# Optimization experiments

Hardware: AMD Instinct MI355X
Metric: run time of the kernel (lower is better)

Reference implementation:

```python
import jax, jax.numpy as jnp
import numpy as np

H = 128          # hidden
L = 4            # num PNA layers
NG = 32          # graphs in the batch
OUT = 12
N_NODES = 30000
N_EDGES = 480000
IN_NODE = 64
IN_EDGE = 16
EPS_BN = 1e-5
EPS_STD = 1e-5
# deg histogram torch.tensor([1,2,3,4,5,6]): cnt_i nodes have degree i
_cnt = np.arange(1.0, 7.0)
AVG_LOG = float((np.log(np.arange(6) + 1.0) * _cnt).sum() / _cnt.sum())


def _lin(k, fan_in, fan_out):
    return jax.random.normal(k, (fan_in, fan_out), jnp.float32) * 0.05


def setup_inputs() -> dict:
    key = jax.random.key(0)
    ks = jax.random.split(key, 16)
    d = {}
    d["x"] = jax.random.normal(ks[0], (N_NODES, IN_NODE), jnp.float32)
    d["edge_attr"] = jax.random.normal(ks[1], (N_EDGES, IN_EDGE), jnp.float32)
    d["edge_index"] = jax.random.randint(ks[2], (2, N_EDGES), 0, N_NODES)
    d["batch"] = jnp.sort(jax.random.randint(ks[3], (N_NODES,), 0, NG))
    d["node_emb_W"] = _lin(ks[4], IN_NODE, H)
    d["node_emb_b"] = jnp.zeros((H,), jnp.float32)
    d["edge_emb_W"] = _lin(ks[5], IN_EDGE, H)
    d["edge_emb_b"] = jnp.zeros((H,), jnp.float32)
    kl = jax.random.split(ks[6], 4 * L)
    d["edge_enc_W"] = jnp.stack([_lin(kl[i], H, H) for i in range(L)])
    d["edge_enc_b"] = jnp.zeros((L, H), jnp.float32)
    d["pre_W"] = jnp.stack([_lin(kl[L + i], 3 * H, H) for i in range(L)])
    d["pre_b"] = jnp.zeros((L, H), jnp.float32)
    d["post_W"] = jnp.stack([_lin(kl[2 * L + i], 13 * H, H) for i in range(L)])
    d["post_b"] = jnp.zeros((L, H), jnp.float32)
    d["lin_W"] = jnp.stack([_lin(kl[3 * L + i], H, H) for i in range(L)])
    d["lin_b"] = jnp.zeros((L, H), jnp.float32)
    d["bn_gamma"] = jnp.ones((L, H), jnp.float32)
    d["bn_beta"] = jnp.zeros((L, H), jnp.float32)
    d["head1_W"] = _lin(ks[7], H, H // 2)
    d["head1_b"] = jnp.zeros((H // 2,), jnp.float32)
    d["head2_W"] = _lin(ks[8], H // 2, OUT)
    d["head2_b"] = jnp.zeros((OUT,), jnp.float32)
    return d


def _pna_layer(x, e, src, dst, eW, eb, pW, pb, oW, ob, lW, lb):
    n = x.shape[0]
    ee = e @ eW + eb                                      # edge encoder [E, H]
    h = jnp.concatenate([x[dst], x[src], ee], axis=-1)    # (x_i, x_j, e) [E, 3H]
    m = h @ pW + pb                                       # pre-nn messages [E, H]
    ones = jnp.ones((m.shape[0],), m.dtype)
    deg = jax.ops.segment_sum(ones, dst, num_segments=n)  # in-degree [N]
    degc = jnp.maximum(deg, 1.0)[:, None]
    has = (deg > 0.0)[:, None]
    mean = jax.ops.segment_sum(m, dst, num_segments=n) / degc
    mn = jnp.where(has, jax.ops.segment_min(m, dst, num_segments=n), 0.0)
    mx = jnp.where(has, jax.ops.segment_max(m, dst, num_segments=n), 0.0)
    mean_sq = jax.ops.segment_sum(m * m, dst, num_segments=n) / degc
    std = jnp.sqrt(jax.nn.relu(mean_sq - mean * mean) + EPS_STD)
    agg = jnp.concatenate([mean, mn, mx, std], axis=-1)   # aggregators [N, 4H]
    amp = jnp.log(degc + 1.0) / AVG_LOG                   # amplification scale
    out = jnp.concatenate([agg, agg * amp, agg / amp], axis=-1)  # id/amp/atten [N, 12H]
    out = jnp.concatenate([x, out], axis=-1) @ oW + ob    # post-nn [N, H]
    return out @ lW + lb                                  # final lin


def reference(x, edge_index, batch, edge_attr, node_emb_W, node_emb_b,
              edge_emb_W, edge_emb_b, edge_enc_W, edge_enc_b, pre_W, pre_b,
              post_W, post_b, lin_W, lin_b, bn_gamma, bn_beta,
              head1_W, head1_b, head2_W, head2_b):
    src, dst = edge_index[0], edge_index[1]
    h = x @ node_emb_W + node_emb_b
    e = edge_attr @ edge_emb_W + edge_emb_b
    for l in range(L):
        h = _pna_layer(h, e, src, dst, edge_enc_W[l], edge_enc_b[l],
                       pre_W[l], pre_b[l], post_W[l], post_b[l],
                       lin_W[l], lin_b[l])
        mu = h.mean(axis=0)
        var = h.var(axis=0)  # biased, as BatchNorm training-mode normalization
        h = (h - mu) / jnp.sqrt(var + EPS_BN) * bn_gamma[l] + bn_beta[l]
        h = jax.nn.relu(h)   # dropout == identity (eval mode reference)
    g = jax.ops.segment_sum(h, batch, num_segments=NG)   # global_add_pool [NG, H]
    z = jax.nn.relu(g @ head1_W + head1_b)
    return z @ head2_W + head2_b
```

## Files before the change

kernel.cpp:

```cpp
#include <hip/hip_runtime.h>
#include <hip/hip_bf16.h>
#include <math.h>

#define NN 30000
#define NE 480000
#define NLAYER 4
#define NGR 32
#define NOUT 12
#define EPS_BN 1e-5f
#define EPS_STD 1e-5f
#define AVG_LOG 1.3821454785305053f

typedef unsigned short ushort_t;
typedef __bf16 bf16x8 __attribute__((ext_vector_type(8)));
typedef float floatx4 __attribute__((ext_vector_type(4)));

__device__ __forceinline__ float bfu(ushort_t u){
  union { unsigned int ui; float f; } c; c.ui = ((unsigned int)u) << 16; return c.f;
}
__device__ __forceinline__ ushort_t f2bf(float f){
  union { float f; unsigned int u; } c; c.f = f;
  unsigned int lsb = (c.u >> 16) & 1u;
  c.u += 0x7FFFu + lsb;
  return (ushort_t)(c.u >> 16);
}

__device__ __forceinline__ int plausible(unsigned int bits32){
  unsigned int e = (bits32 >> 23) & 0xFF;
  if(e == 0xFF) return 0;
  if(bits32 == 0 || bits32 == 0x80000000u) return 1;
  return (e >= 93 && e <= 140) ? 1 : 0;
}

__global__ void k_detect(const ushort_t* __restrict__ xr, int* __restrict__ flag){
  __shared__ int cnt[2];
  if(threadIdx.x < 2) cnt[threadIdx.x] = 0;
  __syncthreads();
  const unsigned int* xf = (const unsigned int*)xr;
  int gf = 0, gb = 0;
  for(int i = threadIdx.x; i < 1024; i += 256){
    gf += plausible(xf[i]);
    gb += plausible(((unsigned int)xr[i]) << 16);
  }
  atomicAdd(&cnt[0], gf);
  atomicAdd(&cnt[1], gb);
  __syncthreads();
  if(threadIdx.x == 0) *flag = (cnt[1] >= cnt[0]) ? 1 : 0;
}

#define NJOBS 19
struct CvtJob { const void* s; float* d; int n; };
struct CvtArgs { CvtJob j[NJOBS]; const int* flag; };

__global__ void k_cvt(CvtArgs a){
  int ji = blockIdx.y;
  const int isbf = *a.flag;
  float* d = a.j[ji].d;
  int n = a.j[ji].n;
  if(isbf){
    const ushort_t* s = (const ushort_t*)a.j[ji].s;
    for(int i = blockIdx.x*256 + threadIdx.x; i < n; i += gridDim.x*256) d[i] = bfu(s[i]);
  } else {
    const float* s = (const float*)a.j[ji].s;
    for(int i = blockIdx.x*256 + threadIdx.x; i < n; i += gridDim.x*256) d[i] = s[i];
  }
}

__global__ void k_xbf(const void* __restrict__ x, ushort_t* __restrict__ d,
                      const int* __restrict__ flag){
  int i = blockIdx.x*256 + threadIdx.x;
  if(i >= NN*64) return;
  if(*flag) d[i] = ((const ushort_t*)x)[i];
  else      d[i] = f2bf(((const float*)x)[i]);
}

#define NTR 29
struct TrJob { const float* s; ushort_t* d; int K, N; };
struct TrArgs { TrJob j[NTR]; };

__global__ void k_tr(TrArgs a){
  TrJob j = a.j[blockIdx.y];
  int total = j.K * j.N;
  for(int i = blockIdx.x*256 + threadIdx.x; i < total; i += gridDim.x*256){
    int n = i / j.K, k = i % j.K;
    j.d[i] = f2bf(j.s[(size_t)k * j.N + n]);
  }
}

__global__ void k_deg(const int* __restrict__ dst, int* __restrict__ deg){
  int i = blockIdx.x*256 + threadIdx.x;
  if(i < NE){
    unsigned d = (unsigned)dst[i];
    if(d < NN) atomicAdd(&deg[d], 1);
  }
}

__global__ void k_scan(const int* __restrict__ deg, int* __restrict__ rp){
  __shared__ int wsum[16];
  __shared__ int carry;
  int tid = threadIdx.x, lane = tid & 63, wid = tid >> 6;
  if(tid==0){ carry = 0; rp[0] = 0; }
  __syncthreads();
  for(int base=0; base<NN; base+=1024){
    int i = base + tid;
    int v = (i<NN) ? deg[i] : 0;
    int incl = v;
    #pragma unroll
    for(int off=1; off<64; off<<=1){
      int t = __shfl_up(incl, off, 64);
      if(lane >= off) incl += t;
    }
    if(lane==63) wsum[wid] = incl;
    __syncthreads();
    int woff = 0;
    for(int wI=0; wI<wid; wI++) woff += wsum[wI];
    if(i<NN) rp[i+1] = carry + woff + incl;
    __syncthreads();
    if(tid==0){
      int t = 0;
      for(int wI=0; wI<16; wI++) t += wsum[wI];
      carry += t;
    }
    __syncthreads();
  }
}

__global__ void k_scatter(const int* __restrict__ src, const int* __restrict__ dst,
                          const int* __restrict__ rp, int* __restrict__ fill,
                          int* __restrict__ src_csr, int* __restrict__ eix_csr){
  int i = blockIdx.x*256 + threadIdx.x;
  if(i >= NE) return;
  unsigned d = (unsigned)dst[i];
  unsigned s = (unsigned)src[i];
  if(d >= NN || s >= NN) return;
  int pos = rp[d] + atomicAdd(&fill[d], 1);
  src_csr[pos] = (int)s;
  eix_csr[pos] = i;
}

__global__ void k_gather_ea(const int* __restrict__ eix, const void* __restrict__ ea,
                            float* __restrict__ out, const int* __restrict__ flag){
  int j = blockIdx.x*128 + threadIdx.x;
  if(j >= NE) return;
  int i = eix[j];
  float* d = out + (size_t)j*16;
  if(*flag){
    const ushort_t* s = (const ushort_t*)ea + (size_t)i*16;
    #pragma unroll
    for(int k=0;k<16;k++) d[k] = bfu(s[k]);
  } else {
    const float* s = (const float*)ea + (size_t)i*16;
    #pragma unroll
    for(int k=0;k<16;k++) d[k] = s[k];
  }
}

__global__ void k_prep_K(const float* __restrict__ embW, const float* __restrict__ embB,
                         const float* __restrict__ encW, const float* __restrict__ encB,
                         const float* __restrict__ preW, const float* __restrict__ preB,
                         float* __restrict__ Kf){
  int l = blockIdx.x, c = threadIdx.x;
  const float* eW = encW + (size_t)l*128*128;
  const float* P3 = preW + (size_t)l*384*128 + 256*128;
  __shared__ float tmp[17][128];
  for(int r=0;r<16;r++){
    float a = 0.f;
    for(int k=0;k<128;k++) a += embW[r*128+k]*eW[k*128+c];
    tmp[r][c] = a;
  }
  {
    float a = encB[l*128+c];
    for(int k=0;k<128;k++) a += embB[k]*eW[k*128+c];
    tmp[16][c] = a;
  }
  __syncthreads();
  float* o = Kf + (size_t)l*17*128;
  for(int r=0;r<16;r++){
    float a = 0.f;
    for(int k=0;k<128;k++) a += tmp[r][k]*P3[k*128+c];
    o[r*128+c] = a;
  }
  {
    float a = preB[l*128+c];
    for(int k=0;k<128;k++) a += tmp[16][k]*P3[k*128+c];
    o[16*128+c] = a;
  }
}

template<int EPI, int OUTBF>
__launch_bounds__(256)
__global__ void k_mm(const ushort_t* __restrict__ A, const ushort_t* __restrict__ BT,
                     void* __restrict__ C, int M, int K, int ldc,
                     const float* __restrict__ bias,
                     const float* __restrict__ Tm,
                     const float* __restrict__ ampv, const float* __restrict__ invv,
                     float* __restrict__ bnsum, float* __restrict__ bnsq){
  __shared__ __align__(16) ushort_t Als[128][88];
  __shared__ __align__(16) ushort_t Bls[128][88];
  __shared__ float s_sum[128];
  __shared__ float s_sq[128];
  const int tid = threadIdx.x;
  const int m0 = blockIdx.x*128, n0 = blockIdx.y*128;
  const int w = tid >> 6, lane = tid & 63;
  const int wm = (w & 1)*64, wn = (w >> 1)*64;
  const int quad = lane >> 4, l15 = lane & 15;
  floatx4 acc[4][4] = {};

  for(int k0=0; k0<K; k0+=64){
    #pragma unroll
    for(int i=0;i<4;i++){
      int c = tid + 256*i;
      int row = c >> 3, kc = (c & 7)*8;
      uint4 va = make_uint4(0u,0u,0u,0u);
      int gr = m0 + row;
      if(gr < M) va = *(const uint4*)(A + (size_t)gr*K + k0 + kc);
      *(uint4*)(&Als[row][kc]) = va;
      uint4 vb = *(const uint4*)(BT + (size_t)(n0+row)*K + k0 + kc);
      *(uint4*)(&Bls[row][kc]) = vb;
    }
    __syncthreads();
    #pragma unroll
    for(int ks=0; ks<64; ks+=32){
      bf16x8 a[4], b[4];
      #pragma unroll
      for(int i=0;i<4;i++) a[i] = *(const bf16x8*)(&Als[wm+16*i+l15][ks+quad*8]);
      #pragma unroll
      for(int j=0;j<4;j++) b[j] = *(const bf16x8*)(&Bls[wn+16*j+l15][ks+quad*8]);
      #pragma unroll
      for(int i=0;i<4;i++)
        #pragma unroll
        for(int j=0;j<4;j++)
          acc[i][j] = __builtin_amdgcn_mfma_f32_16x16x32_bf16(a[i], b[j], acc[i][j], 0, 0, 0);
    }
    __syncthreads();
  }

  float s[4] = {0,0,0,0}, q[4] = {0,0,0,0};
  if(EPI==2){
    if(tid < 128){ s_sum[tid] = 0.f; s_sq[tid] = 0.f; }
    __syncthreads();
  }
  #pragma unroll
  for(int i=0;i<4;i++){
    #pragma unroll
    for(int r=0;r<4;r++){
      int grow = m0 + wm + 16*i + quad*4 + r;
      if(grow >= M) continue;
      float amp = 0.f, iv = 0.f;
      const float* tr = nullptr;
      if(EPI==1){ amp = ampv[grow]; iv = invv[grow]; tr = Tm + (size_t)grow*384; }
      #pragma unroll
      for(int j=0;j<4;j++){
        int gcol = n0 + wn + 16*j + l15;
        float v = acc[i][j][r];
        if(bias) v += bias[gcol];
        if(EPI==1) v += tr[gcol] + amp*tr[128+gcol] + iv*tr[256+gcol];
        if(OUTBF) ((ushort_t*)C)[(size_t)grow*ldc + gcol] = f2bf(v);
        else      ((float*)  C)[(size_t)grow*ldc + gcol] = v;
        if(EPI==2){ s[j] += v; q[j] += v*v; }
      }
    }
  }
  if(EPI==2){
    #pragma unroll
    for(int j=0;j<4;j++){
      atomicAdd(&s_sum[wn + 16*j + l15], s[j]);
      atomicAdd(&s_sq [wn + 16*j + l15], q[j]);
    }
    __syncthreads();
    if(tid < 128){
      atomicAdd(&bnsum[n0 + tid], s_sum[tid]);
      atomicAdd(&bnsq [n0 + tid], s_sq[tid]);
    }
  }
}

__launch_bounds__(128)
__global__ void k_agg(const int* __restrict__ rp, const int* __restrict__ src_csr,
                      const float* __restrict__ ea_csr, const float* __restrict__ Kf,
                      const float* __restrict__ AB,
                      ushort_t* __restrict__ agg, float* __restrict__ ampv,
                      float* __restrict__ invv){
  const int n = blockIdx.x, c = threadIdx.x;
  const int s0 = rp[n], e0 = rp[n+1];
  const int deg = e0 - s0;
  float kcol[16];
  #pragma unroll
  for(int k=0;k<16;k++) kcol[k] = Kf[k*128+c];
  const float base = AB[(size_t)n*256 + c] + Kf[16*128+c];
  float sum=0.f, sq=0.f, mn=INFINITY, mx=-INFINITY;
  __shared__ float ea_s[16][16];
  __shared__ int src_s[16];
  for(int j0=s0; j0<e0; j0+=16){
    int cnt = min(16, e0-j0);
    __syncthreads();
    int ee = c>>4, kk = c&15;
    if(ee < cnt)   ea_s[ee][kk]   = ea_csr[(size_t)(j0+ee)*16+kk];
    if(ee+8 < cnt) ea_s[ee+8][kk] = ea_csr[(size_t)(j0+ee+8)*16+kk];
    if(c < cnt) src_s[c] = src_csr[j0+c];
    __syncthreads();
    for(int e=0;e<cnt;e++){
      float m = base + AB[(size_t)src_s[e]*256 + 128 + c];
      #pragma unroll
      for(int k=0;k<16;k++) m += ea_s[e][k]*kcol[k];
      sum += m; sq += m*m; mn = fminf(mn,m); mx = fmaxf(mx,m);
    }
  }
  float degc = (float)(deg>0?deg:1);
  float mean = sum/degc;
  float var  = fmaxf(sq/degc - mean*mean, 0.f);
  float sd = sqrtf(var + EPS_STD);
  if(deg==0){ mn=0.f; mx=0.f; }
  ushort_t* o = agg + (size_t)n*512;
  o[c]       = f2bf(mean);
  o[128+c]   = f2bf(mn);
  o[256+c]   = f2bf(mx);
  o[384+c]   = f2bf(sd);
  if(c==0){
    float amp = logf(degc+1.f)/AVG_LOG;
    ampv[n] = amp; invv[n] = 1.f/amp;
  }
}

__global__ void k_bn_fin(const float* __restrict__ bnsum, const float* __restrict__ bnsq,
                         const float* __restrict__ gamma, const float* __restrict__ beta,
                         float* __restrict__ scale, float* __restrict__ shift){
  int c = threadIdx.x;
  float mu  = bnsum[c]*(1.f/NN);
  float var = fmaxf(bnsq[c]*(1.f/NN) - mu*mu, 0.f);
  float inv = 1.f/sqrtf(var + EPS_BN);
  float sc = gamma[c]*inv;
  scale[c] = sc;
  shift[c] = beta[c] - mu*sc;
}

__global__ void k_bn_relu(const float* __restrict__ y, const float* __restrict__ scale,
                          const float* __restrict__ shift, ushort_t* __restrict__ h){
  int i = blockIdx.x*256 + threadIdx.x;
  if(i >= NN*128) return;
  int c = i & 127;
  float v = fmaxf(y[i]*scale[c] + shift[c], 0.f);
  h[i] = f2bf(v);
}

__launch_bounds__(128)
__global__ void k_pool(const ushort_t* __restrict__ h, const int* __restrict__ batch,
                       float* __restrict__ g){
  int c = threadIdx.x;
  int r0 = blockIdx.x*512;
  int r1 = min(r0+512, NN);
  int cur = batch[r0] & 31;
  float acc = 0.f;
  for(int r=r0;r<r1;r++){
    int b = batch[r] & 31;
    if(b != cur){ atomicAdd(&g[(size_t)cur*128+c], acc); acc=0.f; cur=b; }
    acc += bfu(h[(size_t)r*128+c]);
  }
  atomicAdd(&g[(size_t)cur*128+c], acc);
}

__launch_bounds__(256)
__global__ void k_head(const float* __restrict__ g, const float* __restrict__ W1,
                       const float* __restrict__ b1, const float* __restrict__ W2,
                       const float* __restrict__ b2, void* __restrict__ out,
                       const int* __restrict__ flag){
  __shared__ float gs[32][128];
  __shared__ float zs[32][64];
  int tid = threadIdx.x;
  for(int i=tid;i<32*128;i+=256) gs[i>>7][i&127] = g[i];
  __syncthreads();
  for(int i=tid;i<32*64;i+=256){
    int r=i>>6, c=i&63;
    float a = b1[c];
    for(int k=0;k<128;k++) a += gs[r][k]*W1[k*64+c];
    zs[r][c] = fmaxf(a, 0.f);
  }
  __syncthreads();
  const int isbf = *flag;
  for(int i=tid;i<NGR*NOUT;i+=256){
    int r = i/NOUT, c = i%NOUT;
    float a = b2[c];
    for(int k=0;k<64;k++) a += zs[r][k]*W2[k*12+c];
    if(isbf) ((ushort_t*)out)[i] = f2bf(a);
    else     ((float*)out)[i] = a;
  }
}

extern "C" void kernel_launch(void* const* d_in, const int* in_sizes, int n_in,
                              void* d_out, int out_size, void* d_ws, size_t ws_size,
                              hipStream_t stream){
  const void* x_raw = d_in[0];
  const void* ea_raw;
  const int*  eidx;
  const int*  batch;
  if(in_sizes[1] == 2*NE){
    eidx   = (const int*)d_in[1];
    batch  = (const int*)d_in[2];
    ea_raw = d_in[3];
  } else {
    ea_raw = d_in[1];
    eidx   = (const int*)d_in[2];
    batch  = (const int*)d_in[3];
  }
  const void* nembW_r = d_in[4];
  const void* nembB_r = d_in[5];
  const void* eembW_r = d_in[6];
  const void* eembB_r = d_in[7];
  const void* encW_r  = d_in[8];
  const void* encB_r  = d_in[9];
  const void* preW_r  = d_in[10];
  const void* preB_r  = d_in[11];
  const void* postW_r = d_in[12];
  const void* postB_r = d_in[13];
  const void* linW_r  = d_in[14];
  const void* linB_r  = d_in[15];
  const void* bnG_r   = d_in[16];
  const void* bnB_r   = d_in[17];
  const void* h1W_r   = d_in[18];
  const void* h1B_r   = d_in[19];
  const void* h2W_r   = d_in[20];
  const void* h2B_r   = d_in[21];

  char* p = (char*)d_ws;
  auto alloc = [&](size_t bytes)->void*{
    void* r = (void*)p; p += (bytes + 255) & ~(size_t)255; return r;
  };
  int*      dtflag  = (int*)     alloc(sizeof(int)*16);
  int*      deg     = (int*)     alloc(sizeof(int)*NN);
  int*      fill    = (int*)     alloc(sizeof(int)*NN);
  int*      rp      = (int*)     alloc(sizeof(int)*(NN+1));
  int*      src_csr = (int*)     alloc(sizeof(int)*NE);
  int*      eix_csr = (int*)     alloc(sizeof(int)*NE);
  float*    ea_csr  = (float*)   alloc(sizeof(float)*(size_t)NE*16);
  ushort_t* xbf     = (ushort_t*)alloc(sizeof(ushort_t)*(size_t)NN*64);
  ushort_t* h       = (ushort_t*)alloc(sizeof(ushort_t)*(size_t)NN*128);
  ushort_t* aggb    = (ushort_t*)alloc(sizeof(ushort_t)*(size_t)NN*512);
  ushort_t* z       = (ushort_t*)alloc(sizeof(ushort_t)*(size_t)NN*128);
  float*    AB      = (float*)   alloc(sizeof(float)*(size_t)NN*256);
  float*    Tm      = (float*)   alloc(sizeof(float)*(size_t)NN*384);
  float*    y       = (float*)   alloc(sizeof(float)*(size_t)NN*128);
  float*    ampv    = (float*)   alloc(sizeof(float)*NN);
  float*    invv    = (float*)   alloc(sizeof(float)*NN);
  float*    Kf      = (float*)   alloc(sizeof(float)*4*17*128);
  float*    bnstat  = (float*)   alloc(sizeof(float)*256);
  float*    bnscale = (float*)   alloc(sizeof(float)*128);
  float*    bnshift = (float*)   alloc(sizeof(float)*128);
  float*    g       = (float*)   alloc(sizeof(float)*32*128);
  ushort_t* WembT   = (ushort_t*)alloc(sizeof(ushort_t)*128*64);
  ushort_t* P12T    = (ushort_t*)alloc(sizeof(ushort_t)*4*256*128);
  ushort_t* WcatT   = (ushort_t*)alloc(sizeof(ushort_t)*(size_t)4*384*512);
  ushort_t* W0T     = (ushort_t*)alloc(sizeof(ushort_t)*4*128*128);
  ushort_t* linWT   = (ushort_t*)alloc(sizeof(ushort_t)*4*128*128);
  float* nembW = (float*)alloc(sizeof(float)*64*128);
  float* nembB = (float*)alloc(sizeof(float)*128);
  float* eembW = (float*)alloc(sizeof(float)*16*128);
  float* eembB = (float*)alloc(sizeof(float)*128);
  float* encW  = (float*)alloc(sizeof(float)*4*128*128);
  float* encB  = (float*)alloc(sizeof(float)*4*128);
  float* preW  = (float*)alloc(sizeof(float)*4*384*128);
  float* preB  = (float*)alloc(sizeof(float)*4*128);
  float* postW = (float*)alloc(sizeof(float)*(size_t)4*1664*128);
  float* postB = (float*)alloc(sizeof(float)*4*128);
  float* linW  = (float*)alloc(sizeof(float)*4*128*128);
  float* linB  = (float*)alloc(sizeof(float)*4*128);
  float* bnG   = (float*)alloc(sizeof(float)*4*128);
  float* bnB   = (float*)alloc(sizeof(float)*4*128);
  float* h1W   = (float*)alloc(sizeof(float)*128*64);
  float* h1B   = (float*)alloc(sizeof(float)*64);
  float* h2W   = (float*)alloc(sizeof(float)*64*12);
  float* h2B   = (float*)alloc(sizeof(float)*12);

  CvtArgs ca;
  ca.flag = dtflag;
  int ji = 0;
  auto job = [&](const void* s, float* d, int n){ ca.j[ji].s=s; ca.j[ji].d=d; ca.j[ji].n=n; ji++; };
  job(nembW_r, nembW, 64*128);
  job(nembB_r, nembB, 128);
  job(eembW_r, eembW, 16*128);
  job(eembB_r, eembB, 128);
  job(encW_r,  encW,  4*128*128);
  job(encB_r,  encB,  4*128);
  job(preW_r,  preW,  4*384*128);
  job(preB_r,  preB,  4*128);
  job(postW_r, postW, 4*1664*128);
  job(postB_r, postB, 4*128);
  job(linW_r,  linW,  4*128*128);
  job(linB_r,  linB,  4*128);
  job(bnG_r,   bnG,   4*128);
  job(bnB_r,   bnB,   4*128);
  job(h1W_r,   h1W,   128*64);
  job(h1B_r,   h1B,   64);
  job(h2W_r,   h2W,   64*12);
  job(h2B_r,   h2B,   12);
  job(h2B_r,   h2B,   12);

  TrArgs ta;
  int ti = 0;
  auto tj = [&](const float* s, ushort_t* d, int K, int N){ ta.j[ti].s=s; ta.j[ti].d=d; ta.j[ti].K=K; ta.j[ti].N=N; ti++; };
  tj(nembW, WembT, 64, 128);
  for(int l=0;l<4;l++){
    const float* pw = preW + (size_t)l*384*128;
    tj(pw,            P12T + (size_t)l*256*128,           128, 128);
    tj(pw + 128*128,  P12T + (size_t)l*256*128 + 128*128, 128, 128);
    const float* po = postW + (size_t)l*1664*128;
    for(int b=0;b<3;b++)
      tj(po + (size_t)(128 + b*512)*128, WcatT + (size_t)l*384*512 + (size_t)b*128*512, 512, 128);
    tj(po, W0T + (size_t)l*128*128, 128, 128);
    tj(linW + (size_t)l*128*128, linWT + (size_t)l*128*128, 128, 128);
  }

  const int* esrc = eidx;
  const int* edst = eidx + NE;

  hipMemsetAsync(deg, 0, sizeof(int)*NN, stream);
  hipMemsetAsync(fill, 0, sizeof(int)*NN, stream);
  hipMemsetAsync(g, 0, sizeof(float)*32*128, stream);

  k_detect<<<1, 256, 0, stream>>>((const ushort_t*)x_raw, dtflag);
  k_cvt<<<dim3(256, NJOBS), 256, 0, stream>>>(ca);
  k_xbf<<<(NN*64+255)/256, 256, 0, stream>>>(x_raw, xbf, dtflag);
  k_tr<<<dim3(32, NTR), 256, 0, stream>>>(ta);

  k_deg<<<(NE+255)/256, 256, 0, stream>>>(edst, deg);
  k_scan<<<1, 1024, 0, stream>>>(deg, rp);
  k_scatter<<<(NE+255)/256, 256, 0, stream>>>(esrc, edst, rp, fill, src_csr, eix_csr);
  k_gather_ea<<<(NE+127)/128, 128, 0, stream>>>(eix_csr, ea_raw, ea_csr, dtflag);
  k_prep_K<<<4, 128, 0, stream>>>(eembW, eembB, encW, encB, preW, preB, Kf);

  const int MB = (NN + 127)/128;

  k_mm<0,1><<<dim3(MB,1), 256, 0, stream>>>(xbf, WembT, h, NN, 64, 128,
                                            nembB, nullptr, nullptr, nullptr, nullptr, nullptr);

  for(int l=0; l<NLAYER; l++){
    k_mm<0,0><<<dim3(MB,2), 256, 0, stream>>>(h, P12T + (size_t)l*256*128, AB, NN, 128, 256,
                                              nullptr, nullptr, nullptr, nullptr, nullptr, nullptr);
    k_agg<<<NN, 128, 0, stream>>>(rp, src_csr, ea_csr, Kf + (size_t)l*17*128,
                                  AB, aggb, ampv, invv);
    k_mm<0,0><<<dim3(MB,3), 256, 0, stream>>>(aggb, WcatT + (size_t)l*384*512, Tm, NN, 512, 384,
                                              nullptr, nullptr, nullptr, nullptr, nullptr, nullptr);
    k_mm<1,1><<<dim3(MB,1), 256, 0, stream>>>(h, W0T + (size_t)l*128*128, z, NN, 128, 128,
                                              postB + l*128, Tm, ampv, invv, nullptr, nullptr);
    hipMemsetAsync(bnstat, 0, sizeof(float)*256, stream);
    k_mm<2,0><<<dim3(MB,1), 256, 0, stream>>>(z, linWT + (size_t)l*128*128, y, NN, 128, 128,
                                              linB + l*128, nullptr, nullptr, nullptr,
                                              bnstat, bnstat+128);
    k_bn_fin<<<1, 128, 0, stream>>>(bnstat, bnstat+128, bnG + l*128, bnB + l*128,
                                    bnscale, bnshift);
    k_bn_relu<<<(NN*128+255)/256, 256, 0, stream>>>(y, bnscale, bnshift, h);
  }

  k_pool<<<(NN+511)/512, 128, 0, stream>>>(h, batch, g);
  k_head<<<1, 256, 0, stream>>>(g, h1W, h1B, h2W, h2B, d_out, dtflag);
}
```

Baseline: 1.194 ms.

## Fold final linear into post weights, drop one GEMM per layer, parallelize setup

The final linear layer is folded into the post-NN weights and bias on the device, which removes one 128x128 GEMM and the intermediate z buffer in every layer. BatchNorm statistics move into the fused epilogue as per-block partial sums, replacing atomics and a memset. Several setup kernels are also restructured: a multi-block prefix scan, a tiled transpose, prep_K split across 68 blocks, pooling without atomics, and edge attributes stored in bf16. A per-node insertion sort keeps the CSR edge order deterministic, and folding the weights changes rounding slightly.

```diff
diff --git a/kernel.cpp b/kernel.cpp
--- a/kernel.cpp
+++ b/kernel.cpp
@@ -10,6 +10,7 @@
 #define EPS_BN 1e-5f
 #define EPS_STD 1e-5f
 #define AVG_LOG 1.3821454785305053f
+#define MB_GRID 235
 
 typedef unsigned short ushort_t;
 typedef __bf16 bf16x8 __attribute__((ext_vector_type(8)));
@@ -48,7 +49,7 @@
   if(threadIdx.x == 0) *flag = (cnt[1] >= cnt[0]) ? 1 : 0;
 }
 
-#define NJOBS 19
+#define NJOBS 18
 struct CvtJob { const void* s; float* d; int n; };
 struct CvtArgs { CvtJob j[NJOBS]; const int* flag; };
 
@@ -74,17 +75,76 @@
   else      d[i] = f2bf(((const float*)x)[i]);
 }
 
-#define NTR 29
+#define NTR 9
 struct TrJob { const float* s; ushort_t* d; int K, N; };
 struct TrArgs { TrJob j[NTR]; };
 
 __global__ void k_tr(TrArgs a){
   TrJob j = a.j[blockIdx.y];
-  int total = j.K * j.N;
-  for(int i = blockIdx.x*256 + threadIdx.x; i < total; i += gridDim.x*256){
-    int n = i / j.K, k = i % j.K;
-    j.d[i] = f2bf(j.s[(size_t)k * j.N + n]);
-  }
+  int nk = j.K >> 6, nn = j.N >> 6;
+  int tile = blockIdx.x;
+  if(tile >= nk*nn) return;
+  int tk = tile % nk, tn = tile / nk;
+  int k0 = tk*64, n0 = tn*64;
+  __shared__ float t[64][65];
+  int w = threadIdx.x >> 6, c = threadIdx.x & 63;
+  #pragma unroll
+  for(int i=0;i<16;i+=1){
+    int r = i*4 + w;
+    t[r][c] = j.s[(size_t)(k0+r)*j.N + n0 + c];
+  }
+  __syncthreads();
+  #pragma unroll
+  for(int i=0;i<16;i+=1){
+    int r = i*4 + w;
+    j.d[(size_t)(n0+r)*j.K + k0 + c] = f2bf(t[c][r]);
+  }
+}
+
+#define NFOLD 16
+struct FoldJob { const float* s1; const float* s2; ushort_t* d; int Kd; };
+struct FoldArgs { FoldJob j[NFOLD]; };
+
+__global__ void k_fold(FoldArgs a){
+  FoldJob j = a.j[blockIdx.y];
+  const int n0 = blockIdx.x*16;
+  __shared__ float s2s[128][16];
+  int tid = threadIdx.x;
+  for(int idx = tid; idx < 128*16; idx += 256){
+    int t = idx >> 4, jj = idx & 15;
+    s2s[t][jj] = j.s2[t*128 + n0 + jj];
+  }
+  __syncthreads();
+  for(int k = tid; k < j.Kd; k += 256){
+    float part[16];
+    #pragma unroll
+    for(int p=0;p<16;p++) part[p] = 0.f;
+    for(int t0=0; t0<128; t0+=32){
+      float rr[32];
+      #pragma unroll
+      for(int tt=0;tt<32;tt++) rr[tt] = j.s1[(size_t)k*128 + t0 + tt];
+      #pragma unroll
+      for(int p=0;p<16;p++){
+        float acc = 0.f;
+        #pragma unroll
+        for(int tt=0;tt<32;tt++) acc += rr[tt]*s2s[t0+tt][p];
+        part[p] += acc;
+      }
+    }
+    #pragma unroll
+    for(int p=0;p<16;p++)
+      j.d[(size_t)(n0+p)*j.Kd + k] = f2bf(part[p]);
+  }
+}
+
+__global__ void k_foldb(const float* __restrict__ postB, const float* __restrict__ linW,
+                        const float* __restrict__ linB, float* __restrict__ biasY){
+  int l = blockIdx.x, c = threadIdx.x;
+  float a = linB[l*128+c];
+  const float* L = linW + (size_t)l*128*128;
+  const float* pb = postB + l*128;
+  for(int t=0;t<128;t++) a += pb[t]*L[t*128+c];
+  biasY[l*128+c] = a;
 }
 
 __global__ void k_deg(const int* __restrict__ dst, int* __restrict__ deg){
@@ -95,34 +155,42 @@
   }
 }
 
-__global__ void k_scan(const int* __restrict__ deg, int* __restrict__ rp){
+__global__ void k_scan1(const int* __restrict__ deg, int* __restrict__ rp,
+                        int* __restrict__ bsum){
   __shared__ int wsum[16];
-  __shared__ int carry;
   int tid = threadIdx.x, lane = tid & 63, wid = tid >> 6;
-  if(tid==0){ carry = 0; rp[0] = 0; }
-  __syncthreads();
-  for(int base=0; base<NN; base+=1024){
-    int i = base + tid;
-    int v = (i<NN) ? deg[i] : 0;
-    int incl = v;
-    #pragma unroll
-    for(int off=1; off<64; off<<=1){
-      int t = __shfl_up(incl, off, 64);
-      if(lane >= off) incl += t;
-    }
-    if(lane==63) wsum[wid] = incl;
-    __syncthreads();
-    int woff = 0;
-    for(int wI=0; wI<wid; wI++) woff += wsum[wI];
-    if(i<NN) rp[i+1] = carry + woff + incl;
-    __syncthreads();
-    if(tid==0){
-      int t = 0;
-      for(int wI=0; wI<16; wI++) t += wsum[wI];
-      carry += t;
-    }
-    __syncthreads();
-  }
+  int i = blockIdx.x*1024 + tid;
+  int v = (i < NN) ? deg[i] : 0;
+  int incl = v;
+  #pragma unroll
+  for(int off=1; off<64; off<<=1){
+    int t = __shfl_up(incl, off, 64);
+    if(lane >= off) incl += t;
+  }
+  if(lane==63) wsum[wid] = incl;
+  __syncthreads();
+  int woff = 0;
+  for(int w=0; w<wid; w++) woff += wsum[w];
+  if(i < NN) rp[i+1] = incl + woff;
+  if(tid == 0){
+    int t = 0;
+    for(int w=0; w<16; w++) t += wsum[w];
+    bsum[blockIdx.x] = t;
+  }
+}
+
+__global__ void k_scan2(const int* __restrict__ bsum, int* __restrict__ boff,
+                        int* __restrict__ rp, int nb){
+  if(threadIdx.x == 0){
+    int run = 0;
+    for(int b=0;b<nb;b++){ boff[b] = run; run += bsum[b]; }
+    rp[0] = 0;
+  }
+}
+
+__global__ void k_scan3(int* __restrict__ rp, const int* __restrict__ boff){
+  int i = blockIdx.x*1024 + threadIdx.x;
+  if(i < NN) rp[i+1] += boff[blockIdx.x];
 }
 
 __global__ void k_scatter(const int* __restrict__ src, const int* __restrict__ dst,
@@ -138,20 +206,36 @@
   eix_csr[pos] = i;
 }
 
+__global__ void k_srt(const int* __restrict__ rp, int* __restrict__ eix,
+                      int* __restrict__ src){
+  int n = blockIdx.x*256 + threadIdx.x;
+  if(n >= NN) return;
+  int s0 = rp[n], e0 = rp[n+1];
+  for(int i=s0+1;i<e0;i++){
+    int ke = eix[i], ks = src[i];
+    int j = i-1;
+    while(j >= s0 && eix[j] > ke){
+      eix[j+1] = eix[j]; src[j+1] = src[j]; j--;
+    }
+    eix[j+1] = ke; src[j+1] = ks;
+  }
+}
+
 __global__ void k_gather_ea(const int* __restrict__ eix, const void* __restrict__ ea,
-                            float* __restrict__ out, const int* __restrict__ flag){
+                            ushort_t* __restrict__ out, const int* __restrict__ flag){
   int j = blockIdx.x*128 + threadIdx.x;
   if(j >= NE) return;
   int i = eix[j];
-  float* d = out + (size_t)j*16;
+  uint4* d = (uint4*)(out + (size_t)j*16);
   if(*flag){
-    const ushort_t* s = (const ushort_t*)ea + (size_t)i*16;
-    #pragma unroll
-    for(int k=0;k<16;k++) d[k] = bfu(s[k]);
+    const uint4* s = (const uint4*)((const ushort_t*)ea + (size_t)i*16);
+    d[0] = s[0]; d[1] = s[1];
   } else {
     const float* s = (const float*)ea + (size_t)i*16;
+    union { ushort_t us[16]; uint4 u4[2]; } pk;
     #pragma unroll
-    for(int k=0;k<16;k++) d[k] = s[k];
+    for(int k=0;k<16;k++) pk.us[k] = f2bf(s[k]);
+    d[0] = pk.u4[0]; d[1] = pk.u4[1];
   }
 }
 
@@ -159,32 +243,26 @@
                          const float* __restrict__ encW, const float* __restrict__ encB,
                          const float* __restrict__ preW, const float* __restrict__ preB,
                          float* __restrict__ Kf){
-  int l = blockIdx.x, c = threadIdx.x;
+  int bx = blockIdx.x;
+  int l = bx / 17, r = bx % 17;
+  int c = threadIdx.x;
   const float* eW = encW + (size_t)l*128*128;
   const float* P3 = preW + (size_t)l*384*128 + 256*128;
-  __shared__ float tmp[17][128];
-  for(int r=0;r<16;r++){
-    float a = 0.f;
-    for(int k=0;k<128;k++) a += embW[r*128+k]*eW[k*128+c];
-    tmp[r][c] = a;
-  }
-  {
-    float a = encB[l*128+c];
+  __shared__ float trow[128];
+  float a;
+  if(r < 16){
+    a = 0.f;
+    const float* w = embW + r*128;
+    for(int k=0;k<128;k++) a += w[k]*eW[k*128+c];
+  } else {
+    a = encB[l*128+c];
     for(int k=0;k<128;k++) a += embB[k]*eW[k*128+c];
-    tmp[16][c] = a;
-  }
-  __syncthreads();
-  float* o = Kf + (size_t)l*17*128;
-  for(int r=0;r<16;r++){
-    float a = 0.f;
-    for(int k=0;k<128;k++) a += tmp[r][k]*P3[k*128+c];
-    o[r*128+c] = a;
-  }
-  {
-    float a = preB[l*128+c];
-    for(int k=0;k<128;k++) a += tmp[16][k]*P3[k*128+c];
-    o[16*128+c] = a;
-  }
+  }
+  trow[c] = a;
+  __syncthreads();
+  float o = (r==16) ? preB[l*128+c] : 0.f;
+  for(int k=0;k<128;k++) o += trow[k]*P3[k*128+c];
+  Kf[(size_t)l*17*128 + r*128 + c] = o;
 }
 
 template<int EPI, int OUTBF>
@@ -194,11 +272,11 @@
                      const float* __restrict__ bias,
                      const float* __restrict__ Tm,
                      const float* __restrict__ ampv, const float* __restrict__ invv,
-                     float* __restrict__ bnsum, float* __restrict__ bnsq){
+                     float* __restrict__ bnpart){
   __shared__ __align__(16) ushort_t Als[128][88];
   __shared__ __align__(16) ushort_t Bls[128][88];
-  __shared__ float s_sum[128];
-  __shared__ float s_sq[128];
+  __shared__ float s_part[8][128];
+  __shared__ float q_part[8][128];
   const int tid = threadIdx.x;
   const int m0 = blockIdx.x*128, n0 = blockIdx.y*128;
   const int w = tid >> 6, lane = tid & 63;
@@ -236,10 +314,6 @@
   }
 
   float s[4] = {0,0,0,0}, q[4] = {0,0,0,0};
-  if(EPI==2){
-    if(tid < 128){ s_sum[tid] = 0.f; s_sq[tid] = 0.f; }
-    __syncthreads();
-  }
   #pragma unroll
   for(int i=0;i<4;i++){
     #pragma unroll
@@ -257,27 +331,31 @@
         if(EPI==1) v += tr[gcol] + amp*tr[128+gcol] + iv*tr[256+gcol];
         if(OUTBF) ((ushort_t*)C)[(size_t)grow*ldc + gcol] = f2bf(v);
         else      ((float*)  C)[(size_t)grow*ldc + gcol] = v;
-        if(EPI==2){ s[j] += v; q[j] += v*v; }
+        if(EPI==1){ s[j] += v; q[j] += v*v; }
       }
     }
   }
-  if(EPI==2){
+  if(EPI==1){
+    const int slot = (w & 1)*4 + quad;
     #pragma unroll
     for(int j=0;j<4;j++){
-      atomicAdd(&s_sum[wn + 16*j + l15], s[j]);
-      atomicAdd(&s_sq [wn + 16*j + l15], q[j]);
+      s_part[slot][wn + 16*j + l15] = s[j];
+      q_part[slot][wn + 16*j + l15] = q[j];
     }
     __syncthreads();
     if(tid < 128){
-      atomicAdd(&bnsum[n0 + tid], s_sum[tid]);
-      atomicAdd(&bnsq [n0 + tid], s_sq[tid]);
+      float ss = 0.f, qq = 0.f;
+      #pragma unroll
+      for(int sl=0; sl<8; sl++){ ss += s_part[sl][tid]; qq += q_part[sl][tid]; }
+      bnpart[(size_t)blockIdx.x*256 + tid]       = ss;
+      bnpart[(size_t)blockIdx.x*256 + 128 + tid] = qq;
     }
   }
 }
 
 __launch_bounds__(128)
 __global__ void k_agg(const int* __restrict__ rp, const int* __restrict__ src_csr,
-                      const float* __restrict__ ea_csr, const float* __restrict__ Kf,
+                      const ushort_t* __restrict__ ea_csr, const float* __restrict__ Kf,
                       const float* __restrict__ AB,
                       ushort_t* __restrict__ agg, float* __restrict__ ampv,
                       float* __restrict__ invv){
@@ -295,8 +373,8 @@
     int cnt = min(16, e0-j0);
     __syncthreads();
     int ee = c>>4, kk = c&15;
-    if(ee < cnt)   ea_s[ee][kk]   = ea_csr[(size_t)(j0+ee)*16+kk];
-    if(ee+8 < cnt) ea_s[ee+8][kk] = ea_csr[(size_t)(j0+ee+8)*16+kk];
+    if(ee < cnt)   ea_s[ee][kk]   = bfu(ea_csr[(size_t)(j0+ee)*16+kk]);
+    if(ee+8 < cnt) ea_s[ee+8][kk] = bfu(ea_csr[(size_t)(j0+ee+8)*16+kk]);
     if(c < cnt) src_s[c] = src_csr[j0+c];
     __syncthreads();
     for(int e=0;e<cnt;e++){
@@ -312,22 +390,27 @@
   float sd = sqrtf(var + EPS_STD);
   if(deg==0){ mn=0.f; mx=0.f; }
   ushort_t* o = agg + (size_t)n*512;
-  o[c]       = f2bf(mean);
-  o[128+c]   = f2bf(mn);
-  o[256+c]   = f2bf(mx);
-  o[384+c]   = f2bf(sd);
+  o[c]     = f2bf(mean);
+  o[128+c] = f2bf(mn);
+  o[256+c] = f2bf(mx);
+  o[384+c] = f2bf(sd);
   if(c==0){
     float amp = logf(degc+1.f)/AVG_LOG;
     ampv[n] = amp; invv[n] = 1.f/amp;
   }
 }
 
-__global__ void k_bn_fin(const float* __restrict__ bnsum, const float* __restrict__ bnsq,
+__global__ void k_bn_fin(const float* __restrict__ bnpart, int nb,
                          const float* __restrict__ gamma, const float* __restrict__ beta,
                          float* __restrict__ scale, float* __restrict__ shift){
   int c = threadIdx.x;
-  float mu  = bnsum[c]*(1.f/NN);
-  float var = fmaxf(bnsq[c]*(1.f/NN) - mu*mu, 0.f);
+  float s = 0.f, q = 0.f;
+  for(int b=0;b<nb;b++){
+    s += bnpart[(size_t)b*256 + c];
+    q += bnpart[(size_t)b*256 + 128 + c];
+  }
+  float mu  = s*(1.f/NN);
+  float var = fmaxf(q*(1.f/NN) - mu*mu, 0.f);
   float inv = 1.f/sqrtf(var + EPS_BN);
   float sc = gamma[c]*inv;
   scale[c] = sc;
@@ -343,46 +426,54 @@
   h[i] = f2bf(v);
 }
 
+__device__ __forceinline__ int lbound(const int* a, int n, int v){
+  int lo = 0, hi = n;
+  while(lo < hi){ int mid = (lo+hi) >> 1; if(a[mid] < v) lo = mid+1; else hi = mid; }
+  return lo;
+}
+
 __launch_bounds__(128)
-__global__ void k_pool(const ushort_t* __restrict__ h, const int* __restrict__ batch,
-                       float* __restrict__ g){
-  int c = threadIdx.x;
-  int r0 = blockIdx.x*512;
-  int r1 = min(r0+512, NN);
-  int cur = batch[r0] & 31;
+__global__ void k_pool1(const ushort_t* __restrict__ h, const int* __restrict__ batch,
+                        float* __restrict__ gpart){
+  int b = blockIdx.x, ch = blockIdx.y, c = threadIdx.x;
+  int lo = lbound(batch, NN, b), hi = lbound(batch, NN, b+1);
+  int len = hi - lo;
+  int per = (len + 7) >> 3;
+  int r0 = min(lo + ch*per, hi);
+  int r1 = min(r0 + per, hi);
   float acc = 0.f;
-  for(int r=r0;r<r1;r++){
-    int b = batch[r] & 31;
-    if(b != cur){ atomicAdd(&g[(size_t)cur*128+c], acc); acc=0.f; cur=b; }
-    acc += bfu(h[(size_t)r*128+c]);
-  }
-  atomicAdd(&g[(size_t)cur*128+c], acc);
-}
-
-__launch_bounds__(256)
+  for(int r=r0;r<r1;r++) acc += bfu(h[(size_t)r*128+c]);
+  gpart[((size_t)b*8 + ch)*128 + c] = acc;
+}
+
+__global__ void k_pool2(const float* __restrict__ gpart, float* __restrict__ g){
+  int b = blockIdx.x, c = threadIdx.x;
+  float acc = 0.f;
+  #pragma unroll
+  for(int ch=0; ch<8; ch++) acc += gpart[((size_t)b*8 + ch)*128 + c];
+  g[(size_t)b*128 + c] = acc;
+}
+
+__launch_bounds__(64)
 __global__ void k_head(const float* __restrict__ g, const float* __restrict__ W1,
                        const float* __restrict__ b1, const float* __restrict__ W2,
                        const float* __restrict__ b2, void* __restrict__ out,
                        const int* __restrict__ flag){
-  __shared__ float gs[32][128];
-  __shared__ float zs[32][64];
-  int tid = threadIdx.x;
-  for(int i=tid;i<32*128;i+=256) gs[i>>7][i&127] = g[i];
-  __syncthreads();
-  for(int i=tid;i<32*64;i+=256){
-    int r=i>>6, c=i&63;
-    float a = b1[c];
-    for(int k=0;k<128;k++) a += gs[r][k]*W1[k*64+c];
-    zs[r][c] = fmaxf(a, 0.f);
-  }
-  __syncthreads();
-  const int isbf = *flag;
-  for(int i=tid;i<NGR*NOUT;i+=256){
-    int r = i/NOUT, c = i%NOUT;
-    float a = b2[c];
-    for(int k=0;k<64;k++) a += zs[r][k]*W2[k*12+c];
-    if(isbf) ((ushort_t*)out)[i] = f2bf(a);
-    else     ((float*)out)[i] = a;
+  __shared__ float gs[128];
+  __shared__ float zs[64];
+  int r = blockIdx.x, tid = threadIdx.x;
+  gs[tid] = g[r*128 + tid];
+  gs[tid+64] = g[r*128 + tid + 64];
+  __syncthreads();
+  float a = b1[tid];
+  for(int k=0;k<128;k++) a += gs[k]*W1[k*64+tid];
+  zs[tid] = fmaxf(a, 0.f);
+  __syncthreads();
+  if(tid < NOUT){
+    float o = b2[tid];
+    for(int k=0;k<64;k++) o += zs[k]*W2[k*12+tid];
+    if(*flag) ((ushort_t*)out)[r*NOUT + tid] = f2bf(o);
+    else      ((float*)out)[r*NOUT + tid] = o;
   }
 }
 
@@ -429,28 +520,30 @@
   int*      deg     = (int*)     alloc(sizeof(int)*NN);
   int*      fill    = (int*)     alloc(sizeof(int)*NN);
   int*      rp      = (int*)     alloc(sizeof(int)*(NN+1));
+  int*      bsum    = (int*)     alloc(sizeof(int)*64);
+  int*      boff    = (int*)     alloc(sizeof(int)*64);
   int*      src_csr = (int*)     alloc(sizeof(int)*NE);
   int*      eix_csr = (int*)     alloc(sizeof(int)*NE);
-  float*    ea_csr  = (float*)   alloc(sizeof(float)*(size_t)NE*16);
+  ushort_t* ea_csr  = (ushort_t*)alloc(sizeof(ushort_t)*(size_t)NE*16);
   ushort_t* xbf     = (ushort_t*)alloc(sizeof(ushort_t)*(size_t)NN*64);
   ushort_t* h       = (ushort_t*)alloc(sizeof(ushort_t)*(size_t)NN*128);
   ushort_t* aggb    = (ushort_t*)alloc(sizeof(ushort_t)*(size_t)NN*512);
-  ushort_t* z       = (ushort_t*)alloc(sizeof(ushort_t)*(size_t)NN*128);
   float*    AB      = (float*)   alloc(sizeof(float)*(size_t)NN*256);
   float*    Tm      = (float*)   alloc(sizeof(float)*(size_t)NN*384);
   float*    y       = (float*)   alloc(sizeof(float)*(size_t)NN*128);
   float*    ampv    = (float*)   alloc(sizeof(float)*NN);
   float*    invv    = (float*)   alloc(sizeof(float)*NN);
   float*    Kf      = (float*)   alloc(sizeof(float)*4*17*128);
-  float*    bnstat  = (float*)   alloc(sizeof(float)*256);
+  float*    bnpart  = (float*)   alloc(sizeof(float)*(size_t)MB_GRID*256);
   float*    bnscale = (float*)   alloc(sizeof(float)*128);
   float*    bnshift = (float*)   alloc(sizeof(float)*128);
+  float*    gpart   = (float*)   alloc(sizeof(float)*32*8*128);
   float*    g       = (float*)   alloc(sizeof(float)*32*128);
+  float*    biasY   = (float*)   alloc(sizeof(float)*4*128);
   ushort_t* WembT   = (ushort_t*)alloc(sizeof(ushort_t)*128*64);
   ushort_t* P12T    = (ushort_t*)alloc(sizeof(ushort_t)*4*256*128);
-  ushort_t* WcatT   = (ushort_t*)alloc(sizeof(ushort_t)*(size_t)4*384*512);
-  ushort_t* W0T     = (ushort_t*)alloc(sizeof(ushort_t)*4*128*128);
-  ushort_t* linWT   = (ushort_t*)alloc(sizeof(ushort_t)*4*128*128);
+  ushort_t* WcatFT  = (ushort_t*)alloc(sizeof(ushort_t)*(size_t)4*384*512);
+  ushort_t* W0FT    = (ushort_t*)alloc(sizeof(ushort_t)*4*128*128);
   float* nembW = (float*)alloc(sizeof(float)*64*128);
   float* nembB = (float*)alloc(sizeof(float)*128);
   float* eembW = (float*)alloc(sizeof(float)*16*128);
@@ -492,7 +585,6 @@
   job(h1B_r,   h1B,   64);
   job(h2W_r,   h2W,   64*12);
   job(h2B_r,   h2B,   12);
-  job(h2B_r,   h2B,   12);
 
   TrArgs ta;
   int ti = 0;
@@ -500,13 +592,27 @@
   tj(nembW, WembT, 64, 128);
   for(int l=0;l<4;l++){
     const float* pw = preW + (size_t)l*384*128;
-    tj(pw,            P12T + (size_t)l*256*128,           128, 128);
-    tj(pw + 128*128,  P12T + (size_t)l*256*128 + 128*128, 128, 128);
+    tj(pw,           P12T + (size_t)l*256*128,           128, 128);
+    tj(pw + 128*128, P12T + (size_t)l*256*128 + 128*128, 128, 128);
+  }
+
+  FoldArgs fa;
+  int fi = 0;
+  for(int l=0;l<4;l++){
     const float* po = postW + (size_t)l*1664*128;
-    for(int b=0;b<3;b++)
-      tj(po + (size_t)(128 + b*512)*128, WcatT + (size_t)l*384*512 + (size_t)b*128*512, 512, 128);
-    tj(po, W0T + (size_t)l*128*128, 128, 128);
-    tj(linW + (size_t)l*128*128, linWT + (size_t)l*128*128, 128, 128);
+    const float* L  = linW + (size_t)l*128*128;
+    for(int b=0;b<3;b++){
+      fa.j[fi].s1 = po + (size_t)(128 + b*512)*128;
+      fa.j[fi].s2 = L;
+      fa.j[fi].d  = WcatFT + (size_t)l*384*512 + (size_t)b*128*512;
+      fa.j[fi].Kd = 512;
+      fi++;
+    }
+    fa.j[fi].s1 = po;
+    fa.j[fi].s2 = L;
+    fa.j[fi].d  = W0FT + (size_t)l*128*128;
+    fa.j[fi].Kd = 128;
+    fi++;
   }
 
   const int* esrc = eidx;
@@ -514,42 +620,41 @@
 
   hipMemsetAsync(deg, 0, sizeof(int)*NN, stream);
   hipMemsetAsync(fill, 0, sizeof(int)*NN, stream);
-  hipMemsetAsync(g, 0, sizeof(float)*32*128, stream);
 
   k_detect<<<1, 256, 0, stream>>>((const ushort_t*)x_raw, dtflag);
-  k_cvt<<<dim3(256, NJOBS), 256, 0, stream>>>(ca);
+  k_cvt<<<dim3(128, NJOBS), 256, 0, stream>>>(ca);
   k_xbf<<<(NN*64+255)/256, 256, 0, stream>>>(x_raw, xbf, dtflag);
-  k_tr<<<dim3(32, NTR), 256, 0, stream>>>(ta);
+  k_tr<<<dim3(4, NTR), 256, 0, stream>>>(ta);
+  k_fold<<<dim3(8, NFOLD), 256, 0, stream>>>(fa);
+  k_foldb<<<4, 128, 0, stream>>>(postB, linW, linB, biasY);
+  k_prep_K<<<68, 128, 0, stream>>>(eembW, eembB, encW, encB, preW, preB, Kf);
 
   k_deg<<<(NE+255)/256, 256, 0, stream>>>(edst, deg);
-  k_scan<<<1, 1024, 0, stream>>>(deg, rp);
+  k_scan1<<<30, 1024, 0, stream>>>(deg, rp, bsum);
+  k_scan2<<<1, 64, 0, stream>>>(bsum, boff, rp, 30);
+  k_scan3<<<30, 1024, 0, stream>>>(rp, boff);
   k_scatter<<<(NE+255)/256, 256, 0, stream>>>(esrc, edst, rp, fill, src_csr, eix_csr);
+  k_srt<<<(NN+255)/256, 256, 0, stream>>>(rp, eix_csr, src_csr);
   k_gather_ea<<<(NE+127)/128, 128, 0, stream>>>(eix_csr, ea_raw, ea_csr, dtflag);
-  k_prep_K<<<4, 128, 0, stream>>>(eembW, eembB, encW, encB, preW, preB, Kf);
-
-  const int MB = (NN + 127)/128;
-
-  k_mm<0,1><<<dim3(MB,1), 256, 0, stream>>>(xbf, WembT, h, NN, 64, 128,
-                                            nembB, nullptr, nullptr, nullptr, nullptr, nullptr);
+
+  k_mm<0,1><<<dim3(MB_GRID,1), 256, 0, stream>>>(xbf, WembT, h, NN, 64, 128,
+                                                 nembB, nullptr, nullptr, nullptr, nullptr);
 
   for(int l=0; l<NLAYER; l++){
-    k_mm<0,0><<<dim3(MB,2), 256, 0, stream>>>(h, P12T + (size_t)l*256*128, AB, NN, 128, 256,
-                                              nullptr, nullptr, nullptr, nullptr, nullptr, nullptr);
+    k_mm<0,0><<<dim3(MB_GRID,2), 256, 0, stream>>>(h, P12T + (size_t)l*256*128, AB, NN, 128, 256,
+                                                   nullptr, nullptr, nullptr, nullptr, nullptr);
     k_agg<<<NN, 128, 0, stream>>>(rp, src_csr, ea_csr, Kf + (size_t)l*17*128,
                                   AB, aggb, ampv, invv);
-    k_mm<0,0><<<dim3(MB,3), 256, 0, stream>>>(aggb, WcatT + (size_t)l*384*512, Tm, NN, 512, 384,
-                                              nullptr, nullptr, nullptr, nullptr, nullptr, nullptr);
-    k_mm<1,1><<<dim3(MB,1), 256, 0, stream>>>(h, W0T + (size_t)l*128*128, z, NN, 128, 128,
-                                              postB + l*128, Tm, ampv, invv, nullptr, nullptr);
-    hipMemsetAsync(bnstat, 0, sizeof(float)*256, stream);
-    k_mm<2,0><<<dim3(MB,1), 256, 0, stream>>>(z, linWT + (size_t)l*128*128, y, NN, 128, 128,
-                                              linB + l*128, nullptr, nullptr, nullptr,
-                                              bnstat, bnstat+128);
-    k_bn_fin<<<1, 128, 0, stream>>>(bnstat, bnstat+128, bnG + l*128, bnB + l*128,
+    k_mm<0,0><<<dim3(MB_GRID,3), 256, 0, stream>>>(aggb, WcatFT + (size_t)l*384*512, Tm, NN, 512, 384,
+                                                   nullptr, nullptr, nullptr, nullptr, nullptr);
+    k_mm<1,0><<<dim3(MB_GRID,1), 256, 0, stream>>>(h, W0FT + (size_t)l*128*128, y, NN, 128, 128,
+                                                   biasY + l*128, Tm, ampv, invv, bnpart);
+    k_bn_fin<<<1, 128, 0, stream>>>(bnpart, MB_GRID, bnG + l*128, bnB + l*128,
                                     bnscale, bnshift);
     k_bn_relu<<<(NN*128+255)/256, 256, 0, stream>>>(y, bnscale, bnshift, h);
   }
 
-  k_pool<<<(NN+511)/512, 128, 0, stream>>>(h, batch, g);
-  k_head<<<1, 256, 0, stream>>>(g, h1W, h1B, h2W, h2B, d_out, dtflag);
-}
+  k_pool1<<<dim3(NGR,8), 128, 0, stream>>>(h, batch, gpart);
+  k_pool2<<<NGR, 128, 0, stream>>>(gpart, g);
+  k_head<<<NGR, 64, 0, stream>>>(g, h1W, h1B, h2W, h2B, d_out, dtflag);
+}
```

Measured after the change: 1.165 ms. 1.02x faster.
